# Kernel optimization log

Measured on AMD Instinct MI355X. Metric: run time of the kernel, lower is better.

## Reference

```python
import jax, jax.numpy as jnp
import numpy as np

EPS = 1e-9
SPREAD_WEIGHT = 0.1
QUAD_WEIGHT = 1.0

N_NODES = 200000
N_EDGES = 12800000
DIM = 128


def to_uhg_space(x):
    # dim > 2: truncate to first 2 features, append homogeneous 1 -> [..., 3]
    ones = jnp.ones((*x.shape[:-1], 1), dtype=x.dtype)
    return jnp.concatenate([x[..., :2], ones], axis=-1)


def uhg_inner(a, b):
    # -<spatial,spatial> + time*time, keepdim
    return -jnp.sum(a[..., :-1] * b[..., :-1], axis=-1, keepdims=True) + a[..., -1:] * b[..., -1:]


def uhg_quadrance(a, b):
    aa = uhg_inner(a, a)
    bb = uhg_inner(b, b)
    ab = uhg_inner(a, b)
    num = ab * ab - aa * bb
    den = aa * bb
    safe = jnp.maximum(jnp.abs(den), EPS) * jnp.sign(den)
    return (num / safe).squeeze(-1)


# spread has the identical formula, applied to lines instead of points
uhg_spread = uhg_quadrance


def setup_inputs() -> dict:
    key = jax.random.key(0)
    k1, k2 = jax.random.split(key)
    z = jax.random.normal(k1, (N_NODES, DIM), dtype=jnp.float32)
    edge_index = jax.random.randint(k2, (2, N_EDGES), 0, N_NODES, dtype=jnp.int32)
    return {"z": z, "edge_index": edge_index}


def reference(z, edge_index):
    z_uhg = to_uhg_space(z)                      # [N, 3]
    src, dst = edge_index[0], edge_index[1]
    # proximity: quadrance over all edges (gather + fused elementwise + mean)
    quad = uhg_quadrance(z_uhg[src], z_uhg[dst])  # [E]
    proximity_loss = quad.mean()
    # compactness: quadrance of every node to the origin [0,0,1]
    origin = jnp.zeros((1, 3), dtype=z.dtype).at[:, -1].set(1.0)
    compactness_loss = uhg_quadrance(z_uhg, origin).mean()
    # lines: vectorized cross product of each point with the origin
    lines = jnp.cross(z_uhg, origin)              # [N, 3]
    # spread over the first min(10, E) edges only (as in the original)
    n_sp = min(10, edge_index.shape[1])
    sp = uhg_spread(lines[src[:n_sp]], lines[dst[:n_sp]])
    spread_loss = sp.mean()
    loss = QUAD_WEIGHT * (proximity_loss + compactness_loss) + SPREAD_WEIGHT * spread_loss
    return loss
```

## Files before the change

kernel.cpp:

```cpp
#include <hip/hip_runtime.h>
#include <hip/hip_bf16.h>

#define UHG_EPS 1e-9
#define ZDIM 128

#define EDGE_BLOCKS 1024
#define NODE_BLOCKS 1024
#define BLOCK 256

#define PART_SHIFT 13
#define PART_SIZE (1 << PART_SHIFT)
#define P_MAX 25
#define NBINS_MAX (P_MAX * P_MAX)
#define STAGE_CAP 56
#define CHUNK 16
#define SCAT_BLOCKS 256
#define SBLOCK 512
#define BBLOCK 1024
#define SENTINEL 0xFFFFFFFFu
#define OVGUARD 4096u

#define PROX_OFF 0
#define COMP_OFF (16 * 1024)
#define GCUR_OFF (24 * 1024)
#define TABLE_OFF (32 * 1024)

typedef float vfloat2 __attribute__((ext_vector_type(2)));
typedef int vint4 __attribute__((ext_vector_type(4)));
typedef unsigned uvec4 __attribute__((ext_vector_type(4)));

__device__ vfloat2 llvm_amdgcn_raw_buffer_load_v2f32(vint4 rsrc, int voffset, int soffset,
                                                     int cpol) __asm("llvm.amdgcn.raw.buffer.load.v2f32");

__device__ __forceinline__ vint4 make_srd(const void* base, unsigned int bytes) {
    union { const void* p; unsigned int w[2]; } pb;
    pb.p = base;
    vint4 r;
    r.x = (int)pb.w[0];
    r.y = (int)pb.w[1];
    r.z = (int)bytes;
    r.w = 0x00020000;
    return r;
}


__device__ __forceinline__ double safe_den(double den) {
    return copysign(fmax(fabs(den), UHG_EPS), den);
}

__device__ __forceinline__ double quad_xy(vfloat2 a, vfloat2 b) {
    double xa = a.x, ya = a.y, xb = b.x, yb = b.y;
    double aa = 1.0 - (xa * xa + ya * ya);
    double bb = 1.0 - (xb * xb + yb * yb);
    double ab = 1.0 - (xa * xb + ya * yb);
    double den = aa * bb;
    double num = ab * ab - den;
    return num / safe_den(den);
}

__device__ __forceinline__ double block_reduce(double v, double* sh) {
    int lane = threadIdx.x & 63;
    int wid = threadIdx.x >> 6;
    v += __shfl_down(v, 32);
    v += __shfl_down(v, 16);
    v += __shfl_down(v, 8);
    v += __shfl_down(v, 4);
    v += __shfl_down(v, 2);
    v += __shfl_down(v, 1);
    if (lane == 0) sh[wid] = v;
    __syncthreads();
    double r = 0.0;
    if (wid == 0) {
        int nw = (int)(blockDim.x >> 6);
        r = (lane < nw) ? sh[lane] : 0.0;
        r += __shfl_down(r, 8);
        r += __shfl_down(r, 4);
        r += __shfl_down(r, 2);
        r += __shfl_down(r, 1);
    }
    __syncthreads();
    return r;
}


__global__ __launch_bounds__(BLOCK) void node_kernel(const float* __restrict__ z,
                                                     vfloat2* __restrict__ table,
                                                     double* __restrict__ comp_partials, int N,
                                                     unsigned* __restrict__ gcur, int nbins) {
    __shared__ double sh[16];
    if (gcur && blockIdx.x == 0) {
        for (int j = threadIdx.x; j < 2 * nbins; j += BLOCK) gcur[j] = 0u;
    }
    const vfloat2* zp = (const vfloat2*)z;
    double local = 0.0;
    for (int i = blockIdx.x * BLOCK + threadIdx.x; i < N; i += NODE_BLOCKS * BLOCK) {
        vfloat2 v = zp[(size_t)i * (ZDIM / 2)];
        if (table) table[i] = v;
        double x = v.x, y = v.y;
        double aa = 1.0 - (x * x + y * y);
        local += (1.0 - aa) / safe_den(aa);
    }
    double tot = block_reduce(local, sh);
    if (threadIdx.x == 0) comp_partials[blockIdx.x] = tot;
}

__global__ __launch_bounds__(SBLOCK) void scatter_kernel(const int* __restrict__ src,
                                                         const int* __restrict__ dst, int E,
                                                         int P, int nbins,
                                                         unsigned* __restrict__ gcur,
                                                         unsigned* __restrict__ gbins,
                                                         int bincap) {
    __shared__ unsigned cnt[NBINS_MAX];
    __shared__ __align__(16) unsigned stage[NBINS_MAX][STAGE_CAP];
    const int tid = threadIdx.x;

    for (int b = tid; b < nbins; b += SBLOCK) cnt[b] = 0u;
    __syncthreads();

#define PROC_EDGE(S, D)                                                                   \
    {                                                                                     \
        int _bin = ((S) >> PART_SHIFT) * P + ((D) >> PART_SHIFT);                         \
        unsigned _val = (unsigned)((S) & (PART_SIZE - 1)) |                               \
                        ((unsigned)((D) & (PART_SIZE - 1)) << PART_SHIFT);                \
        unsigned _slot = atomicAdd(&cnt[_bin], 1u);                                       \
        if (_slot < (unsigned)STAGE_CAP) {                                                \
            stage[_bin][_slot] = _val;                                                    \
        } else {                                                                          \
            unsigned _hp = atomicAdd(&gcur[nbins + _bin], 1u);                            \
            if (_hp < OVGUARD)                                                            \
                gbins[(size_t)_bin * bincap + (bincap - 1 - (int)_hp)] = _val;            \
        }                                                                                 \
    }

    auto flush_bins = [&](bool final_pad) {
        for (int b = tid; b < nbins; b += SBLOCK) {
            unsigned n = cnt[b];
            unsigned m = n < (unsigned)STAGE_CAP ? n : (unsigned)STAGE_CAP;
            while (m >= (unsigned)CHUNK) {
                unsigned pos = atomicAdd(&gcur[b], (unsigned)CHUNK);
                if (pos + CHUNK <= (unsigned)bincap) {
                    unsigned* out = gbins + (size_t)b * bincap + pos;
#pragma unroll
                    for (int j = 0; j < CHUNK / 4; ++j)
                        *(uvec4*)(out + 4 * j) = *(const uvec4*)&stage[b][4 * j];
                } else {
                    for (int j = 0; j < CHUNK; ++j) {
                        unsigned hp = atomicAdd(&gcur[nbins + b], 1u);
                        if (hp < OVGUARD)
                            gbins[(size_t)b * bincap + (bincap - 1 - (int)hp)] = stage[b][j];
                    }
                }
                for (unsigned j = CHUNK; j < m; ++j) stage[b][j - CHUNK] = stage[b][j];
                m -= CHUNK;
            }
            if (final_pad && m > 0) {
                for (unsigned j = m; j < (unsigned)CHUNK; ++j) stage[b][j] = SENTINEL;
                unsigned pos = atomicAdd(&gcur[b], (unsigned)CHUNK);
                if (pos + CHUNK <= (unsigned)bincap) {
                    unsigned* out = gbins + (size_t)b * bincap + pos;
#pragma unroll
                    for (int j = 0; j < CHUNK / 4; ++j)
                        *(uvec4*)(out + 4 * j) = *(const uvec4*)&stage[b][4 * j];
                } else {
                    for (unsigned j = 0; j < m; ++j) {
                        unsigned hp = atomicAdd(&gcur[nbins + b], 1u);
                        if (hp < OVGUARD)
                            gbins[(size_t)b * bincap + (bincap - 1 - (int)hp)] = stage[b][j];
                    }
                }
                m = 0;
            }
            cnt[b] = m;
        }
    };

    long e0 = ((long)blockIdx.x * E / SCAT_BLOCKS) & ~7L;
    long e1 = (blockIdx.x == SCAT_BLOCKS - 1)
                  ? (long)E
                  : (((long)(blockIdx.x + 1) * E / SCAT_BLOCKS) & ~7L);
    long span = e1 - e0;
    long nbatch = span / (8 * SBLOCK);
    long rem0 = e0 + nbatch * 8 * SBLOCK;

    const vint4* s4 = (const vint4*)(src + e0);
    const vint4* d4 = (const vint4*)(dst + e0);

    vint4 cs0 = {}, cs1 = {}, cd0 = {}, cd1 = {};
    if (nbatch > 0) {
        cs0 = __builtin_nontemporal_load(s4 + 2 * tid);
        cs1 = __builtin_nontemporal_load(s4 + 2 * tid + 1);
        cd0 = __builtin_nontemporal_load(d4 + 2 * tid);
        cd1 = __builtin_nontemporal_load(d4 + 2 * tid + 1);
    }
    for (long k = 0; k < nbatch; ++k) {
        vint4 s0 = cs0, s1 = cs1, dd0 = cd0, dd1 = cd1;
        if (k + 1 < nbatch) {
            long b4 = (k + 1) * (2 * SBLOCK) + 2 * tid;
            cs0 = __builtin_nontemporal_load(s4 + b4);
            cs1 = __builtin_nontemporal_load(s4 + b4 + 1);
            cd0 = __builtin_nontemporal_load(d4 + b4);
            cd1 = __builtin_nontemporal_load(d4 + b4 + 1);
        }
        __builtin_amdgcn_sched_barrier(0);
        PROC_EDGE(s0.x, dd0.x);
        PROC_EDGE(s0.y, dd0.y);
        PROC_EDGE(s0.z, dd0.z);
        PROC_EDGE(s0.w, dd0.w);
        PROC_EDGE(s1.x, dd1.x);
        PROC_EDGE(s1.y, dd1.y);
        PROC_EDGE(s1.z, dd1.z);
        PROC_EDGE(s1.w, dd1.w);
        __syncthreads();
        flush_bins(false);
        __syncthreads();
    }
    for (long i = rem0 + tid; i < e1; i += SBLOCK) {
        int s = src[i], d = dst[i];
        PROC_EDGE(s, d);
    }
    __syncthreads();
    flush_bins(true);
#undef PROC_EDGE
}

__global__ __launch_bounds__(BBLOCK) void binned_edge_kernel(const vfloat2* __restrict__ table,
                                                             int N, int P,
                                                             const unsigned* __restrict__ gcur,
                                                             const unsigned* __restrict__ gbins,
                                                             int bincap,
                                                             double* __restrict__ prox_partials) {
    __shared__ vfloat2 pts[2][PART_SIZE];
    __shared__ double sh[16];
    const int bin = blockIdx.x;
    const int sp = bin / P, dp = bin % P;
    const int tid = threadIdx.x;
    const int nbins = P * P;

    for (int j = tid; j < PART_SIZE; j += BBLOCK) {
        int gs = (sp << PART_SHIFT) + j;
        int gd = (dp << PART_SHIFT) + j;
        vfloat2 zv = {0.0f, 0.0f};
        pts[0][j] = (gs < N) ? table[gs] : zv;
        pts[1][j] = (gd < N) ? table[gd] : zv;
    }
    __syncthreads();

    unsigned lo = gcur[bin];
    if (lo > (unsigned)bincap) lo = (unsigned)bincap;
    unsigned hi = gcur[nbins + bin];
    if (hi > OVGUARD) hi = OVGUARD;
    const unsigned* eb = gbins + (size_t)bin * bincap;

    double local = 0.0;
    unsigned i = tid;
    for (; i + 3u * BBLOCK < lo; i += 4u * BBLOCK) {
        unsigned v0 = __builtin_nontemporal_load(eb + i);
        unsigned v1 = __builtin_nontemporal_load(eb + i + BBLOCK);
        unsigned v2 = __builtin_nontemporal_load(eb + i + 2u * BBLOCK);
        unsigned v3 = __builtin_nontemporal_load(eb + i + 3u * BBLOCK);
        vfloat2 a0 = pts[0][v0 & (PART_SIZE - 1u)], b0 = pts[1][(v0 >> PART_SHIFT) & (PART_SIZE - 1u)];
        vfloat2 a1 = pts[0][v1 & (PART_SIZE - 1u)], b1 = pts[1][(v1 >> PART_SHIFT) & (PART_SIZE - 1u)];
        vfloat2 a2 = pts[0][v2 & (PART_SIZE - 1u)], b2 = pts[1][(v2 >> PART_SHIFT) & (PART_SIZE - 1u)];
        vfloat2 a3 = pts[0][v3 & (PART_SIZE - 1u)], b3 = pts[1][(v3 >> PART_SHIFT) & (PART_SIZE - 1u)];
        if (v0 != SENTINEL) local += quad_xy(a0, b0);
        if (v1 != SENTINEL) local += quad_xy(a1, b1);
        if (v2 != SENTINEL) local += quad_xy(a2, b2);
        if (v3 != SENTINEL) local += quad_xy(a3, b3);
    }
    for (; i < lo; i += BBLOCK) {
        unsigned v = eb[i];
        if (v != SENTINEL)
            local += quad_xy(pts[0][v & (PART_SIZE - 1u)],
                             pts[1][(v >> PART_SHIFT) & (PART_SIZE - 1u)]);
    }
    for (unsigned j = tid; j < hi; j += BBLOCK) {
        unsigned v = eb[bincap - 1 - (int)j];
        local += quad_xy(pts[0][v & (PART_SIZE - 1u)],
                         pts[1][(v >> PART_SHIFT) & (PART_SIZE - 1u)]);
    }
    double tot = block_reduce(local, sh);
    if (tid == 0) prox_partials[bin] = tot;
}

#define GATHER8(dsta, i0, i1)                                                   \
    dsta[0] = llvm_amdgcn_raw_buffer_load_v2f32(srd, (i0).x << SHIFT, 0, 1);    \
    dsta[1] = llvm_amdgcn_raw_buffer_load_v2f32(srd, (i0).y << SHIFT, 0, 1);    \
    dsta[2] = llvm_amdgcn_raw_buffer_load_v2f32(srd, (i0).z << SHIFT, 0, 1);    \
    dsta[3] = llvm_amdgcn_raw_buffer_load_v2f32(srd, (i0).w << SHIFT, 0, 1);    \
    dsta[4] = llvm_amdgcn_raw_buffer_load_v2f32(srd, (i1).x << SHIFT, 0, 1);    \
    dsta[5] = llvm_amdgcn_raw_buffer_load_v2f32(srd, (i1).y << SHIFT, 0, 1);    \
    dsta[6] = llvm_amdgcn_raw_buffer_load_v2f32(srd, (i1).z << SHIFT, 0, 1);    \
    dsta[7] = llvm_amdgcn_raw_buffer_load_v2f32(srd, (i1).w << SHIFT, 0, 1);

template <int COMPACT>
__global__ __launch_bounds__(BLOCK) void edge_kernel(const vint4* __restrict__ src4,
                                                     const vint4* __restrict__ dst4, int nvec,
                                                     const int* __restrict__ src,
                                                     const int* __restrict__ dst, int E,
                                                     const void* __restrict__ xy, int N,
                                                     double* __restrict__ prox_partials) {
    __shared__ double sh[16];
    double local = 0.0;
    int tid = blockIdx.x * BLOCK + threadIdx.x;
    const int gstride = EDGE_BLOCKS * BLOCK;
    const int SHIFT = COMPACT ? 3 : 9;

    vint4 srd = make_srd(xy, COMPACT ? (unsigned int)N * 8u : (unsigned int)N * 512u);

    int nvec2 = nvec / 2;
    int v0 = tid;
    bool p0 = v0 < nvec2;
    int v1 = v0 + gstride;
    bool p1 = v1 < nvec2;

    vint4 is0 = {}, is1 = {}, id0 = {}, id1 = {};
    vfloat2 ca[8] = {}, cb[8] = {};
    vfloat2 na[8] = {}, nb[8] = {};

    if (p0) {
        vint4 s0 = __builtin_nontemporal_load(src4 + 2 * (long)v0);
        vint4 s1 = __builtin_nontemporal_load(src4 + 2 * (long)v0 + 1);
        vint4 d0 = __builtin_nontemporal_load(dst4 + 2 * (long)v0);
        vint4 d1 = __builtin_nontemporal_load(dst4 + 2 * (long)v0 + 1);
        GATHER8(ca, s0, s1);
        GATHER8(cb, d0, d1);
    }
    if (p1) {
        is0 = __builtin_nontemporal_load(src4 + 2 * (long)v1);
        is1 = __builtin_nontemporal_load(src4 + 2 * (long)v1 + 1);
        id0 = __builtin_nontemporal_load(dst4 + 2 * (long)v1);
        id1 = __builtin_nontemporal_load(dst4 + 2 * (long)v1 + 1);
    }

    while (p0) {
        if (p1) {
            GATHER8(na, is0, is1);
            GATHER8(nb, id0, id1);
        }
        int v2 = v1 + gstride;
        bool p2 = v2 < nvec2;
        if (p2) {
            is0 = __builtin_nontemporal_load(src4 + 2 * (long)v2);
            is1 = __builtin_nontemporal_load(src4 + 2 * (long)v2 + 1);
            id0 = __builtin_nontemporal_load(dst4 + 2 * (long)v2);
            id1 = __builtin_nontemporal_load(dst4 + 2 * (long)v2 + 1);
        }
        __builtin_amdgcn_sched_barrier(0);
#pragma unroll
        for (int i = 0; i < 8; ++i) local += quad_xy(ca[i], cb[i]);
#pragma unroll
        for (int i = 0; i < 8; ++i) { ca[i] = na[i]; cb[i] = nb[i]; }
        p0 = p1;
        v1 = v2;
        p1 = p2;
    }

    for (int e = 8 * nvec2 + tid; e < E; e += gstride) {
        vfloat2 a = llvm_amdgcn_raw_buffer_load_v2f32(srd, src[e] << SHIFT, 0, 1);
        vfloat2 b = llvm_amdgcn_raw_buffer_load_v2f32(srd, dst[e] << SHIFT, 0, 1);
        local += quad_xy(a, b);
    }
    double tot = block_reduce(local, sh);
    if (threadIdx.x == 0) prox_partials[blockIdx.x] = tot;
}

__global__ __launch_bounds__(BLOCK) void finalize_kernel(const int* __restrict__ src,
                                                         const int* __restrict__ dst,
                                                         const float* __restrict__ z,
                                                         const double* __restrict__ prox_partials,
                                                         int nprox,
                                                         const double* __restrict__ comp_partials,
                                                         float* __restrict__ out, int N, int E) {
    __shared__ double sh[16];
    int t = threadIdx.x;

    double pl = 0.0;
    for (int i = t; i < nprox; i += BLOCK) pl += prox_partials[i];
    double prox = block_reduce(pl, sh);

    double cl = 0.0;
    for (int i = t; i < NODE_BLOCKS; i += BLOCK) cl += comp_partials[i];
    double comp = block_reduce(cl, sh);

    int n_sp = E < 10 ? E : 10;
    double sl = 0.0;
    if (t < n_sp) {
        int s = src[t], d = dst[t];
        double xa = z[(size_t)s * ZDIM], ya = z[(size_t)s * ZDIM + 1];
        double xb = z[(size_t)d * ZDIM], yb = z[(size_t)d * ZDIM + 1];
        double aa = -(ya * ya + xa * xa);
        double bb = -(yb * yb + xb * xb);
        double ab = -(ya * yb + xa * xb);
        double den = aa * bb;
        sl = (ab * ab - den) / safe_den(den);
    }
    double spread = block_reduce(sl, sh);

    if (t == 0) {
        double loss = prox / (double)E + comp / (double)N;
        if (n_sp > 0) loss += 0.1 * (spread / (double)n_sp);
        out[0] = (float)loss;
    }
}


extern "C" void kernel_launch(void* const* d_in, const int* in_sizes, int n_in,
                              void* d_out, int out_size, void* d_ws, size_t ws_size,
                              hipStream_t stream) {
    const float* z = (const float*)d_in[0];
    const int* edge_index = (const int*)d_in[1];
    float* out = (float*)d_out;

    const int N = in_sizes[0] / ZDIM;
    const int E = in_sizes[1] / 2;
    const int* src = edge_index;
    const int* dst = edge_index + (size_t)E;

    double* prox_partials = (double*)((char*)d_ws + PROX_OFF);
    double* comp_partials = (double*)((char*)d_ws + COMP_OFF);
    unsigned* gcur = (unsigned*)((char*)d_ws + GCUR_OFF);
    vfloat2* table = (vfloat2*)((char*)d_ws + TABLE_OFF);
    bool use_table = ws_size >= TABLE_OFF + (size_t)N * sizeof(vfloat2);

    const int P = (N + PART_SIZE - 1) >> PART_SHIFT;
    const int nbins = P * P;
    size_t gbins_off = TABLE_OFF + (((size_t)N * 8 + 255) & ~(size_t)255);
    bool use_binned = false;
    unsigned* gbins = nullptr;
    int bincap = 0;
    if (use_table && P >= 1 && P <= P_MAX && nbins <= NBINS_MAX && E > nbins * 64 &&
        ws_size > gbins_off) {
        int mean = E / nbins;
        int pad = SCAT_BLOCKS * (CHUNK - 1);
        int cap_want = (mean + pad + 2048 + 31) & ~31;
        size_t avail = ws_size - gbins_off;
        int cap_fit = (int)((avail / ((size_t)nbins * 4)) & ~(size_t)31);
        bincap = cap_fit < cap_want ? cap_fit : cap_want;
        if (bincap >= mean + pad + 512) {
            use_binned = true;
            gbins = (unsigned*)((char*)d_ws + gbins_off);
        }
    }

    node_kernel<<<NODE_BLOCKS, BLOCK, 0, stream>>>(z, use_table ? table : nullptr,
                                                   comp_partials,
                                                   N, use_binned ? gcur : nullptr, nbins);

    if (use_binned) {
        scatter_kernel<<<SCAT_BLOCKS, SBLOCK, 0, stream>>>(src, dst, E, P, nbins, gcur, gbins,
                                                           bincap);
        binned_edge_kernel<<<nbins, BBLOCK, 0, stream>>>(table, N, P, gcur, gbins, bincap,
                                                         prox_partials);
        finalize_kernel<<<1, BLOCK, 0, stream>>>(src, dst, z, prox_partials, nbins,
                                                 comp_partials, out, N, E);
    } else {
        int nvec = E / 4;
        if (use_table) {
            edge_kernel<1><<<EDGE_BLOCKS, BLOCK, 0, stream>>>((const vint4*)src,
                                                              (const vint4*)dst, nvec, src, dst,
                                                              E, table, N, prox_partials);
        } else {
            edge_kernel<0><<<EDGE_BLOCKS, BLOCK, 0, stream>>>((const vint4*)src,
                                                              (const vint4*)dst, nvec, src, dst,
                                                              E, z, N, prox_partials);
        }
        finalize_kernel<<<1, BLOCK, 0, stream>>>(src, dst, z, prox_partials, EDGE_BLOCKS,
                                                 comp_partials, out, N, E);
    }
}
```

Before: 296.1 us.

## Halve scatter stage capacity, double scatter blocks, pad bin counters, vectorize bin reads

The scatter kernel now uses half the LDS staging capacity per bin and twice as many blocks, each thread handling 4 edges per batch instead of 8. This should raise occupancy and spread the partitioning work across more workgroups. Global bin cursors are padded to separate cache lines to reduce atomic contention, which moves the table offset. The binned edge kernel reads packed edges as 16-byte vectors with one-ahead prefetching. The trade-off is more frequent flushes, more padding sentinels per bin, and different bin capacity sizing.

```diff
diff --git a/kernel.cpp b/kernel.cpp
--- a/kernel.cpp
+++ b/kernel.cpp
@@ -12,18 +12,20 @@
 #define PART_SIZE (1 << PART_SHIFT)
 #define P_MAX 25
 #define NBINS_MAX (P_MAX * P_MAX)
-#define STAGE_CAP 56
+#define STAGE_CAP 28
 #define CHUNK 16
-#define SCAT_BLOCKS 256
+#define SCAT_BLOCKS 512
 #define SBLOCK 512
+#define EPB 4
 #define BBLOCK 1024
 #define SENTINEL 0xFFFFFFFFu
 #define OVGUARD 4096u
+#define GPAD 16
 
 #define PROX_OFF 0
 #define COMP_OFF (16 * 1024)
 #define GCUR_OFF (24 * 1024)
-#define TABLE_OFF (32 * 1024)
+#define TABLE_OFF (128 * 1024)
 
 typedef float vfloat2 __attribute__((ext_vector_type(2)));
 typedef int vint4 __attribute__((ext_vector_type(4)));
@@ -89,7 +91,7 @@
                                                      unsigned* __restrict__ gcur, int nbins) {
     __shared__ double sh[16];
     if (gcur && blockIdx.x == 0) {
-        for (int j = threadIdx.x; j < 2 * nbins; j += BLOCK) gcur[j] = 0u;
+        for (int j = threadIdx.x; j < 2 * nbins * GPAD; j += BLOCK) gcur[j] = 0u;
     }
     const vfloat2* zp = (const vfloat2*)z;
     double local = 0.0;
@@ -117,19 +119,10 @@
     for (int b = tid; b < nbins; b += SBLOCK) cnt[b] = 0u;
     __syncthreads();
 
-#define PROC_EDGE(S, D)                                                                   \
+#define OVFLOW(B, V)                                                                      \
     {                                                                                     \
-        int _bin = ((S) >> PART_SHIFT) * P + ((D) >> PART_SHIFT);                         \
-        unsigned _val = (unsigned)((S) & (PART_SIZE - 1)) |                               \
-                        ((unsigned)((D) & (PART_SIZE - 1)) << PART_SHIFT);                \
-        unsigned _slot = atomicAdd(&cnt[_bin], 1u);                                       \
-        if (_slot < (unsigned)STAGE_CAP) {                                                \
-            stage[_bin][_slot] = _val;                                                    \
-        } else {                                                                          \
-            unsigned _hp = atomicAdd(&gcur[nbins + _bin], 1u);                            \
-            if (_hp < OVGUARD)                                                            \
-                gbins[(size_t)_bin * bincap + (bincap - 1 - (int)_hp)] = _val;            \
-        }                                                                                 \
+        unsigned _hp = atomicAdd(&gcur[(size_t)(nbins + (B)) * GPAD], 1u);                \
+        if (_hp < OVGUARD) gbins[(size_t)(B) * bincap + (bincap - 1 - (int)_hp)] = (V);   \
     }
 
     auto flush_bins = [&](bool final_pad) {
@@ -137,36 +130,28 @@
             unsigned n = cnt[b];
             unsigned m = n < (unsigned)STAGE_CAP ? n : (unsigned)STAGE_CAP;
             while (m >= (unsigned)CHUNK) {
-                unsigned pos = atomicAdd(&gcur[b], (unsigned)CHUNK);
+                unsigned pos = atomicAdd(&gcur[(size_t)b * GPAD], (unsigned)CHUNK);
                 if (pos + CHUNK <= (unsigned)bincap) {
                     unsigned* out = gbins + (size_t)b * bincap + pos;
 #pragma unroll
                     for (int j = 0; j < CHUNK / 4; ++j)
                         *(uvec4*)(out + 4 * j) = *(const uvec4*)&stage[b][4 * j];
                 } else {
-                    for (int j = 0; j < CHUNK; ++j) {
-                        unsigned hp = atomicAdd(&gcur[nbins + b], 1u);
-                        if (hp < OVGUARD)
-                            gbins[(size_t)b * bincap + (bincap - 1 - (int)hp)] = stage[b][j];
-                    }
+                    for (int j = 0; j < CHUNK; ++j) OVFLOW(b, stage[b][j]);
                 }
                 for (unsigned j = CHUNK; j < m; ++j) stage[b][j - CHUNK] = stage[b][j];
                 m -= CHUNK;
             }
             if (final_pad && m > 0) {
                 for (unsigned j = m; j < (unsigned)CHUNK; ++j) stage[b][j] = SENTINEL;
-                unsigned pos = atomicAdd(&gcur[b], (unsigned)CHUNK);
+                unsigned pos = atomicAdd(&gcur[(size_t)b * GPAD], (unsigned)CHUNK);
                 if (pos + CHUNK <= (unsigned)bincap) {
                     unsigned* out = gbins + (size_t)b * bincap + pos;
 #pragma unroll
                     for (int j = 0; j < CHUNK / 4; ++j)
                         *(uvec4*)(out + 4 * j) = *(const uvec4*)&stage[b][4 * j];
                 } else {
-                    for (unsigned j = 0; j < m; ++j) {
-                        unsigned hp = atomicAdd(&gcur[nbins + b], 1u);
-                        if (hp < OVGUARD)
-                            gbins[(size_t)b * bincap + (bincap - 1 - (int)hp)] = stage[b][j];
-                    }
+                    for (unsigned j = 0; j < m; ++j) OVFLOW(b, stage[b][j]);
                 }
                 m = 0;
             }
@@ -174,53 +159,59 @@
         }
     };
 
-    long e0 = ((long)blockIdx.x * E / SCAT_BLOCKS) & ~7L;
+    long e0 = ((long)blockIdx.x * E / SCAT_BLOCKS) & ~3L;
     long e1 = (blockIdx.x == SCAT_BLOCKS - 1)
                   ? (long)E
-                  : (((long)(blockIdx.x + 1) * E / SCAT_BLOCKS) & ~7L);
+                  : (((long)(blockIdx.x + 1) * E / SCAT_BLOCKS) & ~3L);
     long span = e1 - e0;
-    long nbatch = span / (8 * SBLOCK);
-    long rem0 = e0 + nbatch * 8 * SBLOCK;
+    long nbatch = span / (EPB * SBLOCK);
+    long rem0 = e0 + nbatch * EPB * SBLOCK;
 
     const vint4* s4 = (const vint4*)(src + e0);
     const vint4* d4 = (const vint4*)(dst + e0);
 
-    vint4 cs0 = {}, cs1 = {}, cd0 = {}, cd1 = {};
+    vint4 cs = {}, cd = {};
     if (nbatch > 0) {
-        cs0 = __builtin_nontemporal_load(s4 + 2 * tid);
-        cs1 = __builtin_nontemporal_load(s4 + 2 * tid + 1);
-        cd0 = __builtin_nontemporal_load(d4 + 2 * tid);
-        cd1 = __builtin_nontemporal_load(d4 + 2 * tid + 1);
+        cs = __builtin_nontemporal_load(s4 + tid);
+        cd = __builtin_nontemporal_load(d4 + tid);
     }
     for (long k = 0; k < nbatch; ++k) {
-        vint4 s0 = cs0, s1 = cs1, dd0 = cd0, dd1 = cd1;
+        vint4 s = cs, d = cd;
         if (k + 1 < nbatch) {
-            long b4 = (k + 1) * (2 * SBLOCK) + 2 * tid;
-            cs0 = __builtin_nontemporal_load(s4 + b4);
-            cs1 = __builtin_nontemporal_load(s4 + b4 + 1);
-            cd0 = __builtin_nontemporal_load(d4 + b4);
-            cd1 = __builtin_nontemporal_load(d4 + b4 + 1);
+            cs = __builtin_nontemporal_load(s4 + (k + 1) * SBLOCK + tid);
+            cd = __builtin_nontemporal_load(d4 + (k + 1) * SBLOCK + tid);
         }
         __builtin_amdgcn_sched_barrier(0);
-        PROC_EDGE(s0.x, dd0.x);
-        PROC_EDGE(s0.y, dd0.y);
-        PROC_EDGE(s0.z, dd0.z);
-        PROC_EDGE(s0.w, dd0.w);
-        PROC_EDGE(s1.x, dd1.x);
-        PROC_EDGE(s1.y, dd1.y);
-        PROC_EDGE(s1.z, dd1.z);
-        PROC_EDGE(s1.w, dd1.w);
+        int bn0 = (s.x >> PART_SHIFT) * P + (d.x >> PART_SHIFT);
+        int bn1 = (s.y >> PART_SHIFT) * P + (d.y >> PART_SHIFT);
+        int bn2 = (s.z >> PART_SHIFT) * P + (d.z >> PART_SHIFT);
+        int bn3 = (s.w >> PART_SHIFT) * P + (d.w >> PART_SHIFT);
+        unsigned vl0 = (unsigned)(s.x & (PART_SIZE - 1)) | ((unsigned)(d.x & (PART_SIZE - 1)) << PART_SHIFT);
+        unsigned vl1 = (unsigned)(s.y & (PART_SIZE - 1)) | ((unsigned)(d.y & (PART_SIZE - 1)) << PART_SHIFT);
+        unsigned vl2 = (unsigned)(s.z & (PART_SIZE - 1)) | ((unsigned)(d.z & (PART_SIZE - 1)) << PART_SHIFT);
+        unsigned vl3 = (unsigned)(s.w & (PART_SIZE - 1)) | ((unsigned)(d.w & (PART_SIZE - 1)) << PART_SHIFT);
+        unsigned sl0 = atomicAdd(&cnt[bn0], 1u);
+        unsigned sl1 = atomicAdd(&cnt[bn1], 1u);
+        unsigned sl2 = atomicAdd(&cnt[bn2], 1u);
+        unsigned sl3 = atomicAdd(&cnt[bn3], 1u);
+        if (sl0 < (unsigned)STAGE_CAP) stage[bn0][sl0] = vl0; else OVFLOW(bn0, vl0);
+        if (sl1 < (unsigned)STAGE_CAP) stage[bn1][sl1] = vl1; else OVFLOW(bn1, vl1);
+        if (sl2 < (unsigned)STAGE_CAP) stage[bn2][sl2] = vl2; else OVFLOW(bn2, vl2);
+        if (sl3 < (unsigned)STAGE_CAP) stage[bn3][sl3] = vl3; else OVFLOW(bn3, vl3);
         __syncthreads();
         flush_bins(false);
         __syncthreads();
     }
     for (long i = rem0 + tid; i < e1; i += SBLOCK) {
         int s = src[i], d = dst[i];
-        PROC_EDGE(s, d);
+        int bn = (s >> PART_SHIFT) * P + (d >> PART_SHIFT);
+        unsigned vl = (unsigned)(s & (PART_SIZE - 1)) | ((unsigned)(d & (PART_SIZE - 1)) << PART_SHIFT);
+        unsigned sl = atomicAdd(&cnt[bn], 1u);
+        if (sl < (unsigned)STAGE_CAP) stage[bn][sl] = vl; else OVFLOW(bn, vl);
     }
     __syncthreads();
     flush_bins(true);
-#undef PROC_EDGE
+#undef OVFLOW
 }
 
 __global__ __launch_bounds__(BBLOCK) void binned_edge_kernel(const vfloat2* __restrict__ table,
@@ -245,30 +236,39 @@
     }
     __syncthreads();
 
-    unsigned lo = gcur[bin];
+    unsigned lo = gcur[(size_t)bin * GPAD];
     if (lo > (unsigned)bincap) lo = (unsigned)bincap;
-    unsigned hi = gcur[nbins + bin];
+    unsigned hi = gcur[(size_t)(nbins + bin) * GPAD];
     if (hi > OVGUARD) hi = OVGUARD;
     const unsigned* eb = gbins + (size_t)bin * bincap;
+    const uvec4* eb4 = (const uvec4*)eb;
 
     double local = 0.0;
+    unsigned nv = lo >> 2;
     unsigned i = tid;
-    for (; i + 3u * BBLOCK < lo; i += 4u * BBLOCK) {
-        unsigned v0 = __builtin_nontemporal_load(eb + i);
-        unsigned v1 = __builtin_nontemporal_load(eb + i + BBLOCK);
-        unsigned v2 = __builtin_nontemporal_load(eb + i + 2u * BBLOCK);
-        unsigned v3 = __builtin_nontemporal_load(eb + i + 3u * BBLOCK);
-        vfloat2 a0 = pts[0][v0 & (PART_SIZE - 1u)], b0 = pts[1][(v0 >> PART_SHIFT) & (PART_SIZE - 1u)];
-        vfloat2 a1 = pts[0][v1 & (PART_SIZE - 1u)], b1 = pts[1][(v1 >> PART_SHIFT) & (PART_SIZE - 1u)];
-        vfloat2 a2 = pts[0][v2 & (PART_SIZE - 1u)], b2 = pts[1][(v2 >> PART_SHIFT) & (PART_SIZE - 1u)];
-        vfloat2 a3 = pts[0][v3 & (PART_SIZE - 1u)], b3 = pts[1][(v3 >> PART_SHIFT) & (PART_SIZE - 1u)];
-        if (v0 != SENTINEL) local += quad_xy(a0, b0);
-        if (v1 != SENTINEL) local += quad_xy(a1, b1);
-        if (v2 != SENTINEL) local += quad_xy(a2, b2);
-        if (v3 != SENTINEL) local += quad_xy(a3, b3);
-    }
-    for (; i < lo; i += BBLOCK) {
-        unsigned v = eb[i];
+    bool have = i < nv;
+    uvec4 cur = {};
+    if (have) cur = __builtin_nontemporal_load(eb4 + i);
+    while (have) {
+        unsigned in2 = i + BBLOCK;
+        bool hn = in2 < nv;
+        uvec4 nxt = {};
+        if (hn) nxt = __builtin_nontemporal_load(eb4 + in2);
+        __builtin_amdgcn_sched_barrier(0);
+        vfloat2 a0 = pts[0][cur.x & (PART_SIZE - 1u)], b0 = pts[1][(cur.x >> PART_SHIFT) & (PART_SIZE - 1u)];
+        vfloat2 a1 = pts[0][cur.y & (PART_SIZE - 1u)], b1 = pts[1][(cur.y >> PART_SHIFT) & (PART_SIZE - 1u)];
+        vfloat2 a2 = pts[0][cur.z & (PART_SIZE - 1u)], b2 = pts[1][(cur.z >> PART_SHIFT) & (PART_SIZE - 1u)];
+        vfloat2 a3 = pts[0][cur.w & (PART_SIZE - 1u)], b3 = pts[1][(cur.w >> PART_SHIFT) & (PART_SIZE - 1u)];
+        if (cur.x != SENTINEL) local += quad_xy(a0, b0);
+        if (cur.y != SENTINEL) local += quad_xy(a1, b1);
+        if (cur.z != SENTINEL) local += quad_xy(a2, b2);
+        if (cur.w != SENTINEL) local += quad_xy(a3, b3);
+        cur = nxt;
+        i = in2;
+        have = hn;
+    }
+    for (unsigned j = (nv << 2) + tid; j < lo; j += BBLOCK) {
+        unsigned v = eb[j];
         if (v != SENTINEL)
             local += quad_xy(pts[0][v & (PART_SIZE - 1u)],
                              pts[1][(v >> PART_SHIFT) & (PART_SIZE - 1u)]);
@@ -431,12 +431,12 @@
     if (use_table && P >= 1 && P <= P_MAX && nbins <= NBINS_MAX && E > nbins * 64 &&
         ws_size > gbins_off) {
         int mean = E / nbins;
-        int pad = SCAT_BLOCKS * (CHUNK - 1);
-        int cap_want = (mean + pad + 2048 + 31) & ~31;
+        int cap_want = (mean + 5504) & ~31;
+        int need_min = mean + 5208;
         size_t avail = ws_size - gbins_off;
         int cap_fit = (int)((avail / ((size_t)nbins * 4)) & ~(size_t)31);
         bincap = cap_fit < cap_want ? cap_fit : cap_want;
-        if (bincap >= mean + pad + 512) {
+        if (bincap >= need_min) {
             use_binned = true;
             gbins = (unsigned*)((char*)d_ws + gbins_off);
         }
```

After: 286.4 us. 1.03x faster.
